# Kernel tuning notes

Hardware: AMD Instinct MI355X
Metric: run time of the kernel (lower is better)

## Reference

```python
import jax, jax.numpy as jnp
import numpy as np

N_HEAD = 16
LN_EPS = 1e-5


def _layernorm(x, g, b):
    mu = jnp.mean(x, axis=-1, keepdims=True)
    var = jnp.mean(jnp.square(x - mu), axis=-1, keepdims=True)
    return (x - mu) * jax.lax.rsqrt(var + LN_EPS) * g + b


def setup_inputs() -> dict:
    key = jax.random.key(0)
    ks = jax.random.split(key, 8)
    B, T, C = 2, 2048, 1024
    Dff = 4 * C
    s = 0.02
    return {
        "x": jax.random.normal(ks[0], (B, T, C), jnp.float32),
        "wq": jax.random.normal(ks[1], (C, C), jnp.float32) * s,
        "wk": jax.random.normal(ks[2], (C, C), jnp.float32) * s,
        "wv": jax.random.normal(ks[3], (C, C), jnp.float32) * s,
        "w_proj": jax.random.normal(ks[4], (C, C), jnp.float32) * s,
        "b_proj": jnp.zeros((C,), jnp.float32),
        "w1": jax.random.normal(ks[5], (C, Dff), jnp.float32) * s,
        "b1": jnp.zeros((Dff,), jnp.float32),
        "w2": jax.random.normal(ks[6], (Dff, C), jnp.float32) * s,
        "b2": jnp.zeros((C,), jnp.float32),
        "g1": jnp.ones((C,), jnp.float32),
        "be1": jnp.zeros((C,), jnp.float32),
        "g2": jnp.ones((C,), jnp.float32),
        "be2": jnp.zeros((C,), jnp.float32),
    }


def reference(x, wq, wk, wv, w_proj, b_proj, w1, b1, w2, b2, g1, be1, g2, be2):
    B, T, C = x.shape
    H = N_HEAD
    hd = C // H
    # QKV projections (all heads folded into one matmul each), -> [B,H,T,hd]
    q = (x @ wq).reshape(B, T, H, hd).transpose(0, 2, 1, 3)
    k = (x @ wk).reshape(B, T, H, hd).transpose(0, 2, 1, 3)
    v = (x @ wv).reshape(B, T, H, hd).transpose(0, 2, 1, 3)
    # scaled causal attention; scale = head_size ** -0.5 as in torch source
    scores = jnp.einsum("bhqd,bhkd->bhqk", q, k) * (hd ** -0.5)
    causal = jnp.tril(jnp.ones((T, T), bool))
    scores = jnp.where(causal, scores, jnp.finfo(scores.dtype).min)
    wei = jax.nn.softmax(scores, axis=-1)
    attn = jnp.einsum("bhqk,bhkd->bhqd", wei, v)  # [B,H,T,hd]
    attn = attn.transpose(0, 2, 1, 3).reshape(B, T, C)
    y = attn @ w_proj + b_proj
    # post-LN residuals as in Block.forward
    x = _layernorm(x + y, g1, be1)
    y = jnp.maximum(x @ w1 + b1, 0.0) @ w2 + b2
    x = _layernorm(x + y, g2, be2)
    return x
```

## Files before the change

kernel.cpp:

```cpp
#include <hip/hip_runtime.h>
#include <hip/hip_bf16.h>


typedef __attribute__((ext_vector_type(8))) short bf16x8;
typedef __attribute__((ext_vector_type(4))) float f32x4;
typedef __attribute__((ext_vector_type(4))) short short4v;

__device__ inline short f2bf(float f) {
    __hip_bfloat16 h = __float2bfloat16(f);
    return *reinterpret_cast<short*>(&h);
}


__global__ __launch_bounds__(256) void convert_f2b(const float* __restrict__ in,
                                                   short* __restrict__ out, int n4) {
    int i = blockIdx.x * 256 + threadIdx.x;
    if (i < n4) {
        float4 v = *(const float4*)(in + (size_t)i * 4);
        short4v o = { f2bf(v.x), f2bf(v.y), f2bf(v.z), f2bf(v.w) };
        *(short4v*)(out + (size_t)i * 4) = o;
    }
}

__global__ __launch_bounds__(256) void transpose4_f2b(const float* __restrict__ s0,
                                                      const float* __restrict__ s1,
                                                      const float* __restrict__ s2,
                                                      const float* __restrict__ s3,
                                                      short* __restrict__ d0,
                                                      short* __restrict__ d1,
                                                      short* __restrict__ d2,
                                                      short* __restrict__ d3,
                                                      float scale0) {
    __shared__ short tile[32][33];
    const int z = blockIdx.z;
    const float* in = z == 0 ? s0 : z == 1 ? s1 : z == 2 ? s2 : s3;
    short* out = z == 0 ? d0 : z == 1 ? d1 : z == 2 ? d2 : d3;
    const float scale = z == 0 ? scale0 : 1.0f;
    int c0 = blockIdx.x * 32, r0 = blockIdx.y * 32;
    int tx = threadIdx.x, ty = threadIdx.y;
    for (int i = ty; i < 32; i += 8)
        tile[i][tx] = f2bf(in[(size_t)(r0 + i) * 1024 + c0 + tx] * scale);
    __syncthreads();
    for (int i = ty; i < 32; i += 8)
        out[(size_t)(c0 + i) * 1024 + r0 + tx] = tile[tx][i];
}

__global__ __launch_bounds__(256) void transpose_f2b(const float* __restrict__ in,
                                                     short* __restrict__ out, int R, int C,
                                                     float scale) {
    __shared__ short tile[32][33];
    int c0 = blockIdx.x * 32, r0 = blockIdx.y * 32;
    int tx = threadIdx.x, ty = threadIdx.y;
    for (int i = ty; i < 32; i += 8)
        tile[i][tx] = f2bf(in[(size_t)(r0 + i) * C + c0 + tx] * scale);
    __syncthreads();
    for (int i = ty; i < 32; i += 8)
        out[(size_t)(c0 + i) * R + r0 + tx] = tile[tx][i];
}

template <int BN, int BIAS, int RELU, int OUTBF>
__device__ __forceinline__ void gemm_core(const short* __restrict__ A,
                                          const short* __restrict__ BT,
                                          const float* __restrict__ bias,
                                          void* __restrict__ Cout,
                                          int N, int K, int lda, int ldb,
                                          int gx, int w,
                                          short* As, short* Bs, bool addbias) {
    constexpr int NI = BN / 32;
    const int tid = threadIdx.x;
    const int wid = tid >> 6;
    const int lane = tid & 63;
    const int wr = wid >> 1, wc = wid & 1;
    const int row0 = (w % gx) * 128;
    const int col0 = (w / gx) * BN;
    const int lr = lane & 15;
    const int lk = (lane >> 4) * 8;
    const int sr = lane >> 3;
    const int scs = ((lane & 7) * 8) ^ (sr * 8);
    const int rsw = (lr & 7) * 8;

    f32x4 acc[4][NI] = {};
    for (int k = 0; k < K; k += 64) {
#pragma unroll
        for (int c = 0; c < 4; ++c) {
            const int ch = wid + c * 4;
            const short* ga = A + (size_t)(row0 + ch * 8 + sr) * lda + k + scs;
            __builtin_amdgcn_global_load_lds(
                (const __attribute__((address_space(1))) unsigned int*)ga,
                (__attribute__((address_space(3))) unsigned int*)(As + ch * 512), 16, 0, 0);
        }
#pragma unroll
        for (int c = 0; c < BN / 32; ++c) {
            const int ch = wid + c * 4;
            const short* gb = BT + (size_t)(col0 + ch * 8 + sr) * ldb + k + scs;
            __builtin_amdgcn_global_load_lds(
                (const __attribute__((address_space(1))) unsigned int*)gb,
                (__attribute__((address_space(3))) unsigned int*)(Bs + ch * 512), 16, 0, 0);
        }
        __syncthreads();
#pragma unroll
        for (int kk = 0; kk < 64; kk += 32) {
            const int cof = (kk + lk) ^ rsw;
            bf16x8 a[4], b[NI];
#pragma unroll
            for (int m = 0; m < 4; ++m)
                a[m] = *(const bf16x8*)(As + (wr * 64 + m * 16 + lr) * 64 + cof);
#pragma unroll
            for (int n = 0; n < NI; ++n)
                b[n] = *(const bf16x8*)(Bs + (wc * (BN / 2) + n * 16 + lr) * 64 + cof);
#pragma unroll
            for (int m = 0; m < 4; ++m)
#pragma unroll
                for (int n = 0; n < NI; ++n)
                    acc[m][n] = __builtin_amdgcn_mfma_f32_16x16x32_bf16(a[m], b[n], acc[m][n], 0, 0, 0);
        }
        __syncthreads();
    }
#pragma unroll
    for (int m = 0; m < 4; ++m) {
        int row = row0 + wr * 64 + m * 16 + (lane >> 4) * 4;
#pragma unroll
        for (int n = 0; n < NI; ++n) {
            int col = col0 + wc * (BN / 2) + n * 16 + lr;
            float bv = (BIAS && addbias) ? bias[col] : 0.0f;
#pragma unroll
            for (int r = 0; r < 4; ++r) {
                float v = acc[m][n][r] + bv;
                if (RELU) v = fmaxf(v, 0.0f);
                if (OUTBF)
                    ((short*)Cout)[(size_t)(row + r) * N + col] = f2bf(v);
                else
                    ((float*)Cout)[(size_t)(row + r) * N + col] = v;
            }
        }
    }
}

template <int BN, int BIAS, int RELU, int OUTBF>
__global__ __launch_bounds__(256) void gemm_bt(const short* __restrict__ A,
                                               const short* __restrict__ BT,
                                               const float* __restrict__ bias,
                                               void* __restrict__ Cout,
                                               int N, int K, int lda, int ldb,
                                               void* __restrict__ Cout2) {
    __shared__ short As[128 * 64];
    __shared__ short Bs[BN * 64];
    const int kz = blockIdx.z;
    if (kz) { A += K; BT += K; Cout = Cout2; }
    const int gx = gridDim.x;
    int flat = blockIdx.x + gx * blockIdx.y;
    const int nwg = gx * gridDim.y;
    int w = flat;
    if ((nwg & 7) == 0) {
        const int q = nwg >> 3;
        w = (flat & 7) * q + (flat >> 3);
    }
    gemm_core<BN, BIAS, RELU, OUTBF>(A, BT, bias, Cout, N, K, lda, ldb, gx, w, As, Bs, kz == 0);
}

__global__ __launch_bounds__(256) void gemm_qkv_vt(const short* __restrict__ x_bf,
                                                   const short* __restrict__ wqkT,
                                                   const short* __restrict__ wvT,
                                                   short* __restrict__ qk,
                                                   short* __restrict__ Vt) {
    __shared__ short As[128 * 64];
    __shared__ short Bs[128 * 64];
    int flat = blockIdx.x;
    if (flat < 512) {
        const int w = (flat & 7) * 64 + (flat >> 3);
        gemm_core<128, 0, 0, 1>(x_bf, wqkT, nullptr, qk, 2048, 1024, 1024, 1024, 32, w, As, Bs, false);
    } else {
        flat -= 512;
        const int w = (flat & 7) * 32 + (flat >> 3);
        gemm_core<128, 0, 0, 1>(wvT, x_bf, nullptr, Vt, 4096, 1024, 1024, 1024, 8, w, As, Bs, false);
    }
}

#define ATT_T 2048
#define ATT_QKS 2048
#define ATT_BT 4096

#define LOADK(KF, KB)                                                                     \
    do {                                                                                  \
        const int k0_ = (KB) * 64;                                                        \
        _Pragma("unroll") for (int t = 0; t < 4; ++t) {                                   \
            const size_t krow_ = (size_t)(b * ATT_T + k0_ + 16 * t + lr) * ATT_QKS + h * 64; \
            KF[t][0] = *(const bf16x8*)(Km + krow_ + g * 8);                              \
            KF[t][1] = *(const bf16x8*)(Km + krow_ + 32 + g * 8);                         \
        }                                                                                 \
    } while (0)

#define LOADV(VF, KB)                                                                     \
    do {                                                                                  \
        const int k0_ = (KB) * 64;                                                        \
        _Pragma("unroll") for (int n = 0; n < 4; ++n)                                     \
            _Pragma("unroll") for (int ks = 0; ks < 2; ++ks)                              \
                VF[n][ks] = *(const bf16x8*)(Vt + (size_t)(h * 64 + n * 16 + lr) * ATT_BT + \
                                             b * ATT_T + k0_ + ks * 32 + g * 8);          \
    } while (0)

#define COMPUTE(KF, VF, KB)                                                               \
    do {                                                                                  \
        const int k0_ = (KB) * 64;                                                        \
        const bool edge_ = (KB) == nfull;                                                 \
        _Pragma("unroll") for (int qs = 0; qs < 2; ++qs) {                                \
            f32x4 st[4];                                                                  \
            __builtin_amdgcn_s_setprio(1);                                                \
            _Pragma("unroll") for (int t = 0; t < 4; ++t) {                               \
                f32x4 s = {};                                                             \
                s = __builtin_amdgcn_mfma_f32_16x16x32_bf16(KF[t][0], aq[qs][0], s, 0, 0, 0); \
                s = __builtin_amdgcn_mfma_f32_16x16x32_bf16(KF[t][1], aq[qs][1], s, 0, 0, 0); \
                st[t] = s;                                                                \
            }                                                                             \
            __builtin_amdgcn_s_setprio(0);                                                \
            float v[4][4];                                                                \
            float mx = -3e38f;                                                            \
            if (edge_) {                                                                  \
                _Pragma("unroll") for (int t = 0; t < 4; ++t)                             \
                    _Pragma("unroll") for (int r = 0; r < 4; ++r) {                       \
                        float val = st[t][r];                                             \
                        if (k0_ + 16 * t + g * 4 + r > qrow[qs]) val = -3e38f;            \
                        v[t][r] = val;                                                    \
                        mx = fmaxf(mx, val);                                              \
                    }                                                                     \
            } else {                                                                      \
                _Pragma("unroll") for (int t = 0; t < 4; ++t)                             \
                    _Pragma("unroll") for (int r = 0; r < 4; ++r) {                       \
                        v[t][r] = st[t][r];                                               \
                        mx = fmaxf(mx, st[t][r]);                                         \
                    }                                                                     \
            }                                                                             \
            mx = fmaxf(mx, __shfl_xor(mx, 16));                                           \
            mx = fmaxf(mx, __shfl_xor(mx, 32));                                           \
            if (!__all(mx <= mrun[qs] + 8.0f)) {                                          \
                const float mnew = fmaxf(mrun[qs], mx);                                   \
                const float alpha = exp2f(mrun[qs] - mnew);                               \
                mrun[qs] = mnew;                                                          \
                lrun[qs] *= alpha;                                                        \
                _Pragma("unroll") for (int n = 0; n < 4; ++n)                             \
                    _Pragma("unroll") for (int r = 0; r < 4; ++r) O[qs][n][r] *= alpha;   \
            }                                                                             \
            const float m0 = mrun[qs];                                                    \
            float rs = 0.0f;                                                              \
            _Pragma("unroll") for (int t = 0; t < 4; ++t) {                               \
                short4v pw;                                                               \
                _Pragma("unroll") for (int r = 0; r < 4; ++r) {                           \
                    float p = exp2f(v[t][r] - m0);                                        \
                    rs += p;                                                              \
                    pw[r] = f2bf(p);                                                      \
                }                                                                         \
                *(short4v*)(&Plds[wid][qs][lr][16 * t + g * 4]) = pw;                     \
            }                                                                             \
            rs += __shfl_xor(rs, 16);                                                     \
            rs += __shfl_xor(rs, 32);                                                     \
            lrun[qs] += rs;                                                               \
        }                                                                                 \
        asm volatile("s_waitcnt lgkmcnt(0)" ::: "memory");                                \
        __builtin_amdgcn_sched_barrier(0);                                                \
        __builtin_amdgcn_s_setprio(1);                                                    \
        _Pragma("unroll") for (int qs = 0; qs < 2; ++qs)                                  \
            _Pragma("unroll") for (int ks = 0; ks < 2; ++ks) {                            \
                bf16x8 pf = *(const bf16x8*)(&Plds[wid][qs][lr][ks * 32 + g * 8]);        \
                _Pragma("unroll") for (int n = 0; n < 4; ++n)                             \
                    O[qs][n] = __builtin_amdgcn_mfma_f32_16x16x32_bf16(VF[n][ks], pf, O[qs][n], 0, 0, 0); \
            }                                                                             \
        __builtin_amdgcn_s_setprio(0);                                                    \
    } while (0)

__global__ __launch_bounds__(128) void flash_attn(const short* __restrict__ Q,
                                                  const short* __restrict__ Km,
                                                  const short* __restrict__ Vt,
                                                  short* __restrict__ Oout) {
    const int f = blockIdx.x;
    const int wid = threadIdx.x >> 6;
    const int lane = threadIdx.x & 63;
    const int lr = lane & 15;
    const int g = lane >> 4;
    const int xcd = f & 7;
    const int k = f >> 3;
    const int bh = xcd * 4 + (k & 3);
    const int b = bh >> 4;
    const int h = bh & 15;
    const int pair = (k >> 2) * 2 + wid;

    __shared__ __align__(16) short Plds[2][2][16][72];

#pragma unroll 1
    for (int job = 0; job < 2; ++job) {
        const int s = job ? (63 - pair) : pair;
        const int q0 = s << 5;
        const int qrow[2] = { q0 + lr, q0 + 16 + lr };
        const int nfull = s >> 1;

        bf16x8 aq[2][2];
#pragma unroll
        for (int qs = 0; qs < 2; ++qs)
#pragma unroll
            for (int ds = 0; ds < 2; ++ds)
                aq[qs][ds] = *(const bf16x8*)(Q + (size_t)(b * ATT_T + q0 + qs * 16 + lr) * ATT_QKS +
                                              h * 64 + ds * 32 + g * 8);

        f32x4 O[2][4] = {};
        float mrun[2] = { -1e30f, -1e30f }, lrun[2] = { 0.0f, 0.0f };

        bf16x8 kfA[4][2], kfB[4][2], vf[4][2];
        LOADK(kfA, 0);
        int kb = 0;
        while (true) {
            LOADV(vf, kb);
            if (kb < nfull) LOADK(kfB, kb + 1);
            COMPUTE(kfA, vf, kb);
            ++kb;
            if (kb > nfull) break;
            LOADV(vf, kb);
            if (kb < nfull) LOADK(kfA, kb + 1);
            COMPUTE(kfB, vf, kb);
            ++kb;
            if (kb > nfull) break;
        }

#pragma unroll
        for (int qs = 0; qs < 2; ++qs) {
            const float inv = 1.0f / lrun[qs];
#pragma unroll
            for (int n = 0; n < 4; ++n) {
                short4v ov;
#pragma unroll
                for (int r = 0; r < 4; ++r) ov[r] = f2bf(O[qs][n][r] * inv);
                *(short4v*)(Oout + (size_t)(b * ATT_T + q0 + qs * 16 + lr) * 1024 +
                            h * 64 + n * 16 + g * 4) = ov;
            }
        }
    }
}

__global__ __launch_bounds__(256) void resid_ln(const float* __restrict__ x,
                                                const float* __restrict__ y,
                                                const float* __restrict__ yb,
                                                const float* __restrict__ g,
                                                const float* __restrict__ be,
                                                float* __restrict__ of,
                                                short* __restrict__ ob) {
    const int row = blockIdx.x;
    const int tid = threadIdx.x;
    const size_t base = (size_t)row * 1024 + tid * 4;
    float4 xv = *(const float4*)(x + base);
    float4 yv = *(const float4*)(y + base);
    float h0 = xv.x + yv.x, h1 = xv.y + yv.y, h2 = xv.z + yv.z, h3 = xv.w + yv.w;
    if (yb) {
        float4 bv2 = *(const float4*)(yb + base);
        h0 += bv2.x; h1 += bv2.y; h2 += bv2.z; h3 += bv2.w;
    }
    float s = h0 + h1 + h2 + h3;
    float ss = h0 * h0 + h1 * h1 + h2 * h2 + h3 * h3;
#pragma unroll
    for (int d = 1; d < 64; d <<= 1) {
        s += __shfl_xor(s, d);
        ss += __shfl_xor(ss, d);
    }
    __shared__ float as_[4], ass_[4];
    if ((tid & 63) == 0) { as_[tid >> 6] = s; ass_[tid >> 6] = ss; }
    __syncthreads();
    s = as_[0] + as_[1] + as_[2] + as_[3];
    ss = ass_[0] + ass_[1] + ass_[2] + ass_[3];
    const float mu = s * (1.0f / 1024.0f);
    const float var = ss * (1.0f / 1024.0f) - mu * mu;
    const float rstd = rsqrtf(var + 1e-5f);
    float4 gv = *(const float4*)(g + tid * 4);
    float4 bv = *(const float4*)(be + tid * 4);
    float o0 = (h0 - mu) * rstd * gv.x + bv.x;
    float o1 = (h1 - mu) * rstd * gv.y + bv.y;
    float o2 = (h2 - mu) * rstd * gv.z + bv.z;
    float o3 = (h3 - mu) * rstd * gv.w + bv.w;
    float4 ov = { o0, o1, o2, o3 };
    *(float4*)(of + base) = ov;
    if (ob) {
        short4v obv = { f2bf(o0), f2bf(o1), f2bf(o2), f2bf(o3) };
        *(short4v*)(ob + base) = obv;
    }
}


extern "C" void kernel_launch(void* const* d_in, const int* in_sizes, int n_in,
                              void* d_out, int out_size, void* d_ws, size_t ws_size,
                              hipStream_t stream) {
    const float* x = (const float*)d_in[0];
    const float* wq = (const float*)d_in[1];
    const float* wk = (const float*)d_in[2];
    const float* wv = (const float*)d_in[3];
    const float* wp = (const float*)d_in[4];
    const float* bproj = (const float*)d_in[5];
    const float* w1 = (const float*)d_in[6];
    const float* b1 = (const float*)d_in[7];
    const float* w2 = (const float*)d_in[8];
    const float* b2 = (const float*)d_in[9];
    const float* g1 = (const float*)d_in[10];
    const float* be1 = (const float*)d_in[11];
    const float* g2 = (const float*)d_in[12];
    const float* be2 = (const float*)d_in[13];

    char* ws = (char*)d_ws;
    const size_t MB = 1024 * 1024;
    short* x_bf = (short*)(ws + 0);
    short* wqkT = (short*)(ws + 8 * MB);
    short* wqT = wqkT;
    short* wkT = (short*)(ws + 10 * MB);
    short* wvT = (short*)(ws + 12 * MB);
    short* w1T = (short*)(ws + 16 * MB);
    short* w2T = (short*)(ws + 24 * MB);
    short* qk  = (short*)(ws + 32 * MB);
    short* wpT = (short*)(ws + 48 * MB);
    short* Vt  = (short*)(ws + 56 * MB);
    short* hbf = (short*)(ws + 32 * MB);
    short* attn = (short*)(ws + 64 * MB);
    short* x1bf = (short*)(ws + 64 * MB);
    float* y1a = (float*)(ws + 72 * MB);
    float* y1b = (float*)(ws + 0);
    float* y2a = (float*)(ws + 72 * MB);
    float* y2b = (float*)(ws + 0);
    float* x1f = (float*)(ws + 88 * MB);

    dim3 blk(256);
    dim3 tb(32, 8);
    const float SC = 0.125f * 1.44269504089f;

    convert_f2b<<<dim3(4096), blk, 0, stream>>>(x, x_bf, 4096 * 1024 / 4);
    transpose4_f2b<<<dim3(32, 32, 4), tb, 0, stream>>>(wq, wk, wv, wp, wqT, wkT, wvT, wpT, SC);
    transpose_f2b<<<dim3(128, 32), tb, 0, stream>>>(w1, w1T, 1024, 4096, 1.0f);
    transpose_f2b<<<dim3(32, 128), tb, 0, stream>>>(w2, w2T, 4096, 1024, 1.0f);

    gemm_qkv_vt<<<dim3(768), blk, 0, stream>>>(x_bf, wqkT, wvT, qk, Vt);
    flash_attn<<<dim3(512), dim3(128), 0, stream>>>(qk, qk + 1024, Vt, attn);
    gemm_bt<64, 1, 0, 0><<<dim3(32, 16, 2), blk, 0, stream>>>(attn, wpT, bproj, y1a,
                                                              1024, 512, 1024, 1024, y1b);
    resid_ln<<<dim3(4096), blk, 0, stream>>>(x, y1a, y1b, g1, be1, x1f, x1bf);
    gemm_bt<128, 1, 1, 1><<<dim3(32, 32), blk, 0, stream>>>(x1bf, w1T, b1, hbf,
                                                            4096, 1024, 1024, 1024, nullptr);
    gemm_bt<64, 1, 0, 0><<<dim3(32, 16, 2), blk, 0, stream>>>(hbf, w2T, b2, y2a,
                                                              1024, 2048, 4096, 4096, y2b);
    resid_ln<<<dim3(4096), blk, 0, stream>>>(x1f, y2a, y2b, g2, be2, (float*)d_out, nullptr);
}
```

Measured before the change: 295.1 us.

## Split attention KV range across two waves and merge partial softmax via LDS

Each workgroup's two waves now work on the same 32-row query tile, each covering half of the causal KV blocks, instead of separate query tiles. Wave 1 writes its partial O, running max and running sum to shared memory, and wave 0 rescales and merges both before writing the output. The grid doubles to keep the total work count, which gives more workgroups and more even per-wave work. The cost is an extra __syncthreads, shared-memory traffic for the merge, and wave 1 sitting idle during the final output.

```diff
diff --git a/kernel.cpp b/kernel.cpp
--- a/kernel.cpp
+++ b/kernel.cpp
@@ -281,9 +281,11 @@
     const int bh = xcd * 4 + (k & 3);
     const int b = bh >> 4;
     const int h = bh & 15;
-    const int pair = (k >> 2) * 2 + wid;
+    const int pair = k >> 2;
 
     __shared__ __align__(16) short Plds[2][2][16][72];
+    __shared__ float slabO[2][32][64];
+    __shared__ float slabML[2][4][64];
 
 #pragma unroll 1
     for (int job = 0; job < 2; ++job) {
@@ -291,6 +293,10 @@
         const int q0 = s << 5;
         const int qrow[2] = { q0 + lr, q0 + 16 + lr };
         const int nfull = s >> 1;
+        const int P = nfull + 1;
+        const int mid = P >> 1;
+        const int lo = wid ? mid : 0;
+        const int hi = wid ? nfull : mid - 1;
 
         bf16x8 aq[2][2];
 #pragma unroll
@@ -304,31 +310,57 @@
         float mrun[2] = { -1e30f, -1e30f }, lrun[2] = { 0.0f, 0.0f };
 
         bf16x8 kfA[4][2], kfB[4][2], vf[4][2];
-        LOADK(kfA, 0);
-        int kb = 0;
-        while (true) {
-            LOADV(vf, kb);
-            if (kb < nfull) LOADK(kfB, kb + 1);
-            COMPUTE(kfA, vf, kb);
-            ++kb;
-            if (kb > nfull) break;
-            LOADV(vf, kb);
-            if (kb < nfull) LOADK(kfA, kb + 1);
-            COMPUTE(kfB, vf, kb);
-            ++kb;
-            if (kb > nfull) break;
-        }
-
-#pragma unroll
-        for (int qs = 0; qs < 2; ++qs) {
-            const float inv = 1.0f / lrun[qs];
-#pragma unroll
-            for (int n = 0; n < 4; ++n) {
-                short4v ov;
-#pragma unroll
-                for (int r = 0; r < 4; ++r) ov[r] = f2bf(O[qs][n][r] * inv);
-                *(short4v*)(Oout + (size_t)(b * ATT_T + q0 + qs * 16 + lr) * 1024 +
-                            h * 64 + n * 16 + g * 4) = ov;
+        if (lo <= hi) {
+            LOADK(kfA, lo);
+            int kb = lo;
+            while (true) {
+                LOADV(vf, kb);
+                if (kb < hi) LOADK(kfB, kb + 1);
+                COMPUTE(kfA, vf, kb);
+                ++kb;
+                if (kb > hi) break;
+                LOADV(vf, kb);
+                if (kb < hi) LOADK(kfA, kb + 1);
+                COMPUTE(kfB, vf, kb);
+                ++kb;
+                if (kb > hi) break;
+            }
+        }
+
+        if (wid == 1) {
+#pragma unroll
+            for (int qs = 0; qs < 2; ++qs) {
+#pragma unroll
+                for (int n = 0; n < 4; ++n)
+#pragma unroll
+                    for (int r = 0; r < 4; ++r)
+                        slabO[job][qs * 16 + n * 4 + r][lane] = O[qs][n][r];
+                slabML[job][qs * 2 + 0][lane] = mrun[qs];
+                slabML[job][qs * 2 + 1][lane] = lrun[qs];
+            }
+        }
+        __syncthreads();
+        if (wid == 0) {
+#pragma unroll
+            for (int qs = 0; qs < 2; ++qs) {
+                const float m1 = slabML[job][qs * 2 + 0][lane];
+                const float l1 = slabML[job][qs * 2 + 1][lane];
+                const float ms = fmaxf(mrun[qs], m1);
+                const float a0 = exp2f(mrun[qs] - ms);
+                const float a1 = exp2f(m1 - ms);
+                const float inv = 1.0f / (lrun[qs] * a0 + l1 * a1);
+#pragma unroll
+                for (int n = 0; n < 4; ++n) {
+                    short4v ov;
+#pragma unroll
+                    for (int r = 0; r < 4; ++r) {
+                        float val = (O[qs][n][r] * a0 +
+                                     slabO[job][qs * 16 + n * 4 + r][lane] * a1) * inv;
+                        ov[r] = f2bf(val);
+                    }
+                    *(short4v*)(Oout + (size_t)(b * ATT_T + q0 + qs * 16 + lr) * 1024 +
+                                h * 64 + n * 16 + g * 4) = ov;
+                }
             }
         }
     }
@@ -430,7 +462,7 @@
     transpose_f2b<<<dim3(32, 128), tb, 0, stream>>>(w2, w2T, 4096, 1024, 1.0f);
 
     gemm_qkv_vt<<<dim3(768), blk, 0, stream>>>(x_bf, wqkT, wvT, qk, Vt);
-    flash_attn<<<dim3(512), dim3(128), 0, stream>>>(qk, qk + 1024, Vt, attn);
+    flash_attn<<<dim3(1024), dim3(128), 0, stream>>>(qk, qk + 1024, Vt, attn);
     gemm_bt<64, 1, 0, 0><<<dim3(32, 16, 2), blk, 0, stream>>>(attn, wpT, bproj, y1a,
                                                               1024, 512, 1024, 1024, y1b);
     resid_ln<<<dim3(4096), blk, 0, stream>>>(x, y1a, y1b, g1, be1, x1f, x1bf);
```

After: 303.2 us. 2.8% more time.
